# Kernel tuning notes

Hardware: AMD Instinct MI355X
Metric: run time of the kernel (lower is better)

The kernel has to match this reference:

```python
import jax, jax.numpy as jnp
import numpy as np

N_ITERS = 150   # unrolled projected-subgradient iterations of the convex DRO program
LR0 = 0.05      # initial step size (decays as 1/sqrt(k))


def project_simplex(v):
    """Euclidean projection of v onto the probability simplex {z >= 0, sum z = 1}."""
    n = v.shape[0]
    u = jnp.sort(v)[::-1]
    css = jnp.cumsum(u)
    idx = jnp.arange(1, n + 1, dtype=v.dtype)
    rho = jnp.sum(u + (1.0 - css) / idx > 0)
    theta = (css[rho - 1] - 1.0) / rho.astype(v.dtype)
    return jnp.maximum(v - theta, 0.0)


def dro_solve(ep, y_hat, delta, gamma):
    """Solve the TV-DRO portfolio problem (Ben-Tal et al. 2013 tractable dual):
        min_{z in simplex, c, eta, lam>=0}
            eta + delta*lam + (1/T) sum_t max(-lam, (ep_t@z - c)^2 - eta) - gamma * y_hat@z
    via unrolled projected subgradient descent (differentiable solver layer).
    """
    n_obs, n_y = ep.shape

    def objective(params):
        z, c, eta, lam = params
        r = ep @ z - c                       # (n_obs,) residual portfolio returns
        m = jnp.maximum(-lam, r * r - eta)   # TV phi-conjugate term
        return eta + delta * lam + jnp.mean(m) - gamma * jnp.dot(y_hat, z)

    grad_fn = jax.grad(objective)
    init = (jnp.full((n_y,), 1.0 / n_y, dtype=ep.dtype),
            jnp.zeros((), ep.dtype), jnp.zeros((), ep.dtype),
            jnp.asarray(0.1, ep.dtype))

    def step(params, k):
        g = grad_fn(params)
        lr = LR0 / jnp.sqrt(1.0 + k)
        z, c, eta, lam = [p - lr * gi for p, gi in zip(params, g)]
        z = project_simplex(z)
        lam = jnp.maximum(lam, 0.0)
        return (z, c, eta, lam), None

    (z, _, _, _), _ = jax.lax.scan(step, init, jnp.arange(N_ITERS, dtype=ep.dtype))
    return z


def setup_inputs() -> dict:
    key = jax.random.key(0)
    k1, k2, k3, k4 = jax.random.split(key, 4)
    n_obs, n_x, n_y = 256, 64, 128
    X = jax.random.normal(k1, (n_obs, n_x), dtype=jnp.float32)
    Y = 0.05 * jax.random.normal(k2, (n_obs, n_y), dtype=jnp.float32)
    W = jax.random.normal(k3, (n_y, n_x), dtype=jnp.float32) / np.sqrt(n_x)
    b = 0.01 * jax.random.normal(k4, (n_y,), dtype=jnp.float32)
    delta = jnp.asarray(0.1, jnp.float32)
    gamma = jnp.asarray(0.1, jnp.float32)
    return {"X": X, "Y": Y, "W": W, "b": b, "delta": delta, "gamma": gamma}


def reference(X, Y, W, b, delta, gamma):
    Y_hat = X @ W.T + b            # pred_layer applied to each x_t (batched)
    ep = Y - Y_hat                 # (n_obs, n_y) residuals
    # One DRO solve per scenario y_hat_t, all sharing the same residual matrix ep.
    Z_star = jax.vmap(lambda yh: dro_solve(ep, yh, delta, gamma))(Y_hat)
    return Z_star, Y_hat
```

## Files before the change

### kernel.cpp

```cpp
#include <hip/hip_runtime.h>
#include <math.h>

#define T_OBS 256
#define NY 128
#define NITER 150

#define DPP_ROW_SHR1 0x111
#define DPP_ROW_SHR2 0x112
#define DPP_ROW_SHR4 0x114
#define DPP_ROW_SHR8 0x118
#define DPP_BCAST15  0x142
#define DPP_BCAST31  0x143

#define DPP_ADD_F32(x, ctrl) \
    (x) += __int_as_float(__builtin_amdgcn_update_dpp(0, __float_as_int(x), (ctrl), 0xf, 0xf, true))

__device__ __forceinline__ void wave_sum2(float& a, float& b) {
    DPP_ADD_F32(a, DPP_ROW_SHR1); DPP_ADD_F32(b, DPP_ROW_SHR1);
    DPP_ADD_F32(a, DPP_ROW_SHR2); DPP_ADD_F32(b, DPP_ROW_SHR2);
    DPP_ADD_F32(a, DPP_ROW_SHR4); DPP_ADD_F32(b, DPP_ROW_SHR4);
    DPP_ADD_F32(a, DPP_ROW_SHR8); DPP_ADD_F32(b, DPP_ROW_SHR8);
    DPP_ADD_F32(a, DPP_BCAST15);  DPP_ADD_F32(b, DPP_BCAST15);
    DPP_ADD_F32(a, DPP_BCAST31);  DPP_ADD_F32(b, DPP_BCAST31);
    a = __int_as_float(__builtin_amdgcn_readlane(__float_as_int(a), 63));
    b = __int_as_float(__builtin_amdgcn_readlane(__float_as_int(b), 63));
}

__device__ __forceinline__ float rl(float x, int l) {
    return __int_as_float(__builtin_amdgcn_readlane(__float_as_int(x), l));
}

__global__ __launch_bounds__(128)
void pred_kernel(const float* __restrict__ X, const float* __restrict__ Y,
                 const float* __restrict__ W, const float* __restrict__ b,
                 float* __restrict__ yhat, float* __restrict__ ep) {
    __shared__ float xrow[64];
    const int t = blockIdx.x;
    const int j = threadIdx.x;
    if (j < 64) xrow[j] = X[t * 64 + j];
    __syncthreads();
    const float* wr = W + j * 64;
    float acc = 0.f;
#pragma unroll
    for (int x = 0; x < 64; ++x) acc = fmaf(xrow[x], wr[x], acc);
    const float yh = acc + b[j];
    yhat[t * NY + j] = yh;
    ep[t * NY + j] = Y[t * NY + j] - yh;
}

__global__ __launch_bounds__(256, 1)
void dro_kernel(const float* __restrict__ ep_g, const float* __restrict__ yhat_g,
                float* __restrict__ z_out,
                const float* __restrict__ d_delta, const float* __restrict__ d_gamma) {
    __shared__ float gzp[2][4][NY];
    __shared__ __align__(16) float red[2][8];

    const int tid  = threadIdx.x;
    const int lane = tid & 63;
    const int wid  = tid >> 6;
    const int blk  = blockIdx.x;

    float4 rA[32];
    {
        const float4* eg4 = (const float4*)ep_g + tid * 32;
#pragma unroll
        for (int q = 0; q < 32; ++q) rA[q] = eg4[q];
    }

    const int j0    = lane << 1;
    const int tbase = wid << 6;
    float2 rB[64];
#pragma unroll
    for (int tt = 0; tt < 64; ++tt)
        rB[tt] = *(const float2*)(ep_g + (tbase + tt) * NY + j0);

    const float yh0 = yhat_g[blk * NY + j0];
    const float yh1 = yhat_g[blk * NY + j0 + 1];

    float z0 = 1.0f / 128.0f, z1 = 1.0f / 128.0f;
    float act0 = 1.f, act1 = 1.f;

    const float delta = d_delta[0];
    const float gamma = d_gamma[0];
    float c = 0.f, eta = 0.f, lam = 0.1f;
    int buf = 0;

    for (int k = 0; k < NITER; ++k) {
        const float lr = 0.05f * __builtin_amdgcn_rsqf(1.0f + (float)k);

        float a0 = 0.f, a1 = 0.f, a2 = 0.f, a3 = 0.f;
#pragma unroll
        for (int q = 0; q < 32; ++q) {
            const float4 e = rA[q];
            const float za = rl(z0, 2 * q);
            const float zb = rl(z1, 2 * q);
            const float zc = rl(z0, 2 * q + 1);
            const float zd = rl(z1, 2 * q + 1);
            a0 = fmaf(e.x, za, a0);
            a1 = fmaf(e.y, zb, a1);
            a2 = fmaf(e.z, zc, a2);
            a3 = fmaf(e.w, zd, a3);
        }
        const float r  = (a0 + a1) + (a2 + a3) - c;
        const float q2 = r * r - eta;
        const float aa = -lam;
        const float st = (q2 > aa) ? 1.0f : ((q2 == aa) ? 0.5f : 0.0f);
        const float wv = st * r;

        float s1 = st, s2 = wv;
        wave_sum2(s1, s2);
        if (lane == 0) { red[buf][wid * 2] = s1; red[buf][wid * 2 + 1] = s2; }

        float p0 = 0.f, p1 = 0.f, p2 = 0.f, p3 = 0.f;
#pragma unroll
        for (int tt = 0; tt < 64; tt += 2) {
            const float wa = rl(wv, tt);
            const float wb = rl(wv, tt + 1);
            const float2 ea = rB[tt];
            const float2 eb = rB[tt + 1];
            p0 = fmaf(wa, ea.x, p0);
            p1 = fmaf(wa, ea.y, p1);
            p2 = fmaf(wb, eb.x, p2);
            p3 = fmaf(wb, eb.y, p3);
        }
        *(float2*)&gzp[buf][wid][j0] = make_float2(p0 + p2, p1 + p3);

        __syncthreads();

        const float4 rd0 = *(const float4*)&red[buf][0];
        const float4 rd1 = *(const float4*)&red[buf][4];
        const float S1 = (rd0.x + rd0.z) + (rd1.x + rd1.z);
        const float S2 = (rd0.y + rd0.w) + (rd1.y + rd1.w);
        c   -= lr * (-(2.0f / 256.0f) * S2);
        eta -= lr * (1.0f - S1 * (1.0f / 256.0f));
        lam  = fmaxf(lam - lr * (delta - 1.0f + S1 * (1.0f / 256.0f)), 0.0f);

        const float2 g0v = *(const float2*)&gzp[buf][0][j0];
        const float2 g1v = *(const float2*)&gzp[buf][1][j0];
        const float2 g2v = *(const float2*)&gzp[buf][2][j0];
        const float2 g3v = *(const float2*)&gzp[buf][3][j0];
        const float g0 = (g0v.x + g1v.x) + (g2v.x + g3v.x);
        const float g1 = (g0v.y + g1v.y) + (g2v.y + g3v.y);
        const float v0 = z0 - lr * ((2.0f / 256.0f) * g0 - gamma * yh0);
        const float v1 = z1 - lr * ((2.0f / 256.0f) * g1 - gamma * yh1);

        float theta = 0.f;
        for (int m = 0; m < 64; ++m) {
            float s  = act0 * v0 + act1 * v1;
            float cc = act0 + act1;
            wave_sum2(s, cc);
            theta = (s - 1.0f) * __builtin_amdgcn_rcpf(cc);
            const float n0 = (v0 > theta) ? 1.0f : 0.0f;
            const float n1 = (v1 > theta) ? 1.0f : 0.0f;
            const bool changed = (n0 != act0) || (n1 != act1);
            act0 = n0; act1 = n1;
            if (!__any(changed)) break;
        }
        z0 = fmaxf(v0 - theta, 0.f);
        z1 = fmaxf(v1 - theta, 0.f);

        buf ^= 1;
    }

    if (wid == 0) *(float2*)&z_out[blk * NY + j0] = make_float2(z0, z1);
}

extern "C" void kernel_launch(void* const* d_in, const int* in_sizes, int n_in,
                              void* d_out, int out_size, void* d_ws, size_t ws_size,
                              hipStream_t stream) {
    const float* X       = (const float*)d_in[0];
    const float* Y       = (const float*)d_in[1];
    const float* W       = (const float*)d_in[2];
    const float* b       = (const float*)d_in[3];
    const float* d_delta = (const float*)d_in[4];
    const float* d_gamma = (const float*)d_in[5];

    float* z_out    = (float*)d_out;
    float* yhat_out = z_out + T_OBS * NY;
    float* ep_ws    = (float*)d_ws;

    pred_kernel<<<T_OBS, 128, 0, stream>>>(X, Y, W, b, yhat_out, ep_ws);
    dro_kernel<<<T_OBS, 256, 0, stream>>>(ep_ws, yhat_out, z_out, d_delta, d_gamma);
}
```

Baseline: 227.3 us.

## Fuse prediction and DRO solver kernels with a global grid barrier

Merges the prediction kernel into the DRO solver kernel. Each block computes its own row of y_hat and ep, then all blocks meet at a software grid barrier built on an atomic counter before loading the full ep matrix. This removes one kernel launch and the gap between the two kernels. The barrier assumes all 256 blocks are resident at the same time, which holds on MI355X's 256 CUs at one block per CU. If they are not all resident it can deadlock, and a block that arrives late stalls every other block.

```diff
diff --git a/kernel.cpp b/kernel.cpp
--- a/kernel.cpp
+++ b/kernel.cpp
@@ -30,39 +30,53 @@
     return __int_as_float(__builtin_amdgcn_readlane(__float_as_int(x), l));
 }
 
-__global__ __launch_bounds__(128)
-void pred_kernel(const float* __restrict__ X, const float* __restrict__ Y,
-                 const float* __restrict__ W, const float* __restrict__ b,
-                 float* __restrict__ yhat, float* __restrict__ ep) {
-    __shared__ float xrow[64];
-    const int t = blockIdx.x;
-    const int j = threadIdx.x;
-    if (j < 64) xrow[j] = X[t * 64 + j];
-    __syncthreads();
-    const float* wr = W + j * 64;
-    float acc = 0.f;
-#pragma unroll
-    for (int x = 0; x < 64; ++x) acc = fmaf(xrow[x], wr[x], acc);
-    const float yh = acc + b[j];
-    yhat[t * NY + j] = yh;
-    ep[t * NY + j] = Y[t * NY + j] - yh;
-}
+__device__ unsigned g_sync = 0u;
 
 __global__ __launch_bounds__(256, 1)
-void dro_kernel(const float* __restrict__ ep_g, const float* __restrict__ yhat_g,
-                float* __restrict__ z_out,
-                const float* __restrict__ d_delta, const float* __restrict__ d_gamma) {
+void fused_kernel(const float* __restrict__ X, const float* __restrict__ Y,
+                  const float* __restrict__ W, const float* __restrict__ b,
+                  float* __restrict__ yhat_out, float* __restrict__ z_out,
+                  float* __restrict__ ep_ws,
+                  const float* __restrict__ d_delta, const float* __restrict__ d_gamma) {
     __shared__ float gzp[2][4][NY];
     __shared__ __align__(16) float red[2][8];
+    __shared__ float xrow[64];
+    __shared__ float yhat_lds[NY];
 
     const int tid  = threadIdx.x;
     const int lane = tid & 63;
     const int wid  = tid >> 6;
     const int blk  = blockIdx.x;
 
+    if (tid < 64) xrow[tid] = X[blk * 64 + tid];
+    __syncthreads();
+    if (tid < NY) {
+        const float* wr = W + tid * 64;
+        float acc = 0.f;
+#pragma unroll
+        for (int x = 0; x < 64; ++x) acc = fmaf(xrow[x], wr[x], acc);
+        const float yh = acc + b[tid];
+        yhat_out[blk * NY + tid] = yh;
+        yhat_lds[tid] = yh;
+        ep_ws[blk * NY + tid] = Y[blk * NY + tid] - yh;
+    }
+    __syncthreads();
+
+    if (tid == 0) {
+        __threadfence();
+        const unsigned old    = atomicAdd(&g_sync, 1u);
+        const unsigned target = (old & ~255u) + 256u;
+        while (__hip_atomic_load(&g_sync, __ATOMIC_RELAXED,
+                                 __HIP_MEMORY_SCOPE_AGENT) < target) {
+            __builtin_amdgcn_s_sleep(2);
+        }
+        __threadfence();
+    }
+    __syncthreads();
+
     float4 rA[32];
     {
-        const float4* eg4 = (const float4*)ep_g + tid * 32;
+        const float4* eg4 = (const float4*)ep_ws + tid * 32;
 #pragma unroll
         for (int q = 0; q < 32; ++q) rA[q] = eg4[q];
     }
@@ -72,10 +86,10 @@
     float2 rB[64];
 #pragma unroll
     for (int tt = 0; tt < 64; ++tt)
-        rB[tt] = *(const float2*)(ep_g + (tbase + tt) * NY + j0);
+        rB[tt] = *(const float2*)(ep_ws + (tbase + tt) * NY + j0);
 
-    const float yh0 = yhat_g[blk * NY + j0];
-    const float yh1 = yhat_g[blk * NY + j0 + 1];
+    const float yh0 = yhat_lds[j0];
+    const float yh1 = yhat_lds[j0 + 1];
 
     float z0 = 1.0f / 128.0f, z1 = 1.0f / 128.0f;
     float act0 = 1.f, act1 = 1.f;
@@ -179,6 +193,6 @@
     float* yhat_out = z_out + T_OBS * NY;
     float* ep_ws    = (float*)d_ws;
 
-    pred_kernel<<<T_OBS, 128, 0, stream>>>(X, Y, W, b, yhat_out, ep_ws);
-    dro_kernel<<<T_OBS, 256, 0, stream>>>(ep_ws, yhat_out, z_out, d_delta, d_gamma);
+    fused_kernel<<<T_OBS, 256, 0, stream>>>(X, Y, W, b, yhat_out, z_out,
+                                            ep_ws, d_delta, d_gamma);
 }
```

Result: slower. 268.9 us (+18.3%).
